# Kernel tuning notes

Hardware: AMD Instinct MI355X
Metric: run time of the kernel (lower is better)

The kernel has to match this reference:

```python
import jax, jax.numpy as jnp
import numpy as np

V, BLK, L, H, C, FF = 50257, 2048, 6, 8, 512, 2048
D = C // H  # head_dim = 64

def setup_inputs() -> dict:
    key = jax.random.key(0)
    ks = jax.random.split(key, 16)
    s = 0.02
    proj_std = 0.02 / np.sqrt(2 * L)
    return {
        'idx': jax.random.randint(ks[0], (2, 2048), 0, V, dtype=jnp.int64),
        'wte': jax.random.normal(ks[1], (V, C), jnp.float32) * s,
        'wpe': jax.random.normal(ks[2], (BLK, C), jnp.float32) * s,
        'ln1_w': jnp.ones((L, C), jnp.float32), 'ln1_b': jnp.zeros((L, C), jnp.float32),
        'c_attn_w': jax.random.normal(ks[3], (L, 3 * C, C), jnp.float32) * s,
        'c_proj_w': jax.random.normal(ks[4], (L, C, C), jnp.float32) * proj_std,
        'ln2_w': jnp.ones((L, C), jnp.float32), 'ln2_b': jnp.zeros((L, C), jnp.float32),
        'fc_w': jax.random.normal(ks[5], (L, FF, C), jnp.float32) * s,
        'proj_w': jax.random.normal(ks[6], (L, C, FF), jnp.float32) * proj_std,
        'lnf_w': jnp.ones((C,), jnp.float32), 'lnf_b': jnp.zeros((C,), jnp.float32),
    }

def _layernorm(x, w, b, eps=1e-5):
    mu = jnp.mean(x, axis=-1, keepdims=True)
    var = jnp.var(x, axis=-1, keepdims=True)
    return (x - mu) * jax.lax.rsqrt(var + eps) * w + b

def _attn(x, attn_w, proj_w, mask):
    B, T, _ = x.shape
    qkv = jnp.einsum('btc,fc->btf', x, attn_w)  # (B,T,3C)
    q, k, v = jnp.split(qkv, 3, axis=-1)
    q = q.reshape(B, T, H, D)
    k = k.reshape(B, T, H, D)
    v = v.reshape(B, T, H, D)
    scale = 1.0 / np.sqrt(D)
    att = jnp.einsum('bthd,bshd->bhts', q, k) * scale  # (B,H,T,T)
    att = jnp.where(mask, att, -jnp.inf)
    att = jax.nn.softmax(att, axis=-1)
    y = jnp.einsum('bhts,bshd->bthd', att, v).reshape(B, T, C)
    return jnp.einsum('btc,oc->bto', y, proj_w)

def reference(idx, wte, wpe, ln1_w, ln1_b, c_attn_w, c_proj_w, ln2_w, ln2_b, fc_w, proj_w, lnf_w, lnf_b):
    B, T = idx.shape
    pos = jnp.arange(T)
    x = wte[idx] + wpe[pos]  # (B,T,C); dropout p=0
    mask = jnp.tril(jnp.ones((T, T), bool))[None, None]
    for i in range(L):
        x = x + _attn(_layernorm(x, ln1_w[i], ln1_b[i]), c_attn_w[i], c_proj_w[i], mask)
        h = _layernorm(x, ln2_w[i], ln2_b[i])
        h = jax.nn.gelu(jnp.einsum('btc,fc->btf', h, fc_w[i]), approximate=False)
        x = x + jnp.einsum('btf,cf->btc', h, proj_w[i])
    x = _layernorm(x, lnf_w, lnf_b)
    logits = jnp.einsum('btc,vc->btv', x, wte)  # tied lm_head
    return logits
```

## Files before the change

### kernel.cpp

```cpp
#include <hip/hip_runtime.h>

typedef unsigned short u16;
typedef short bf16x8 __attribute__((ext_vector_type(8)));
typedef float f32x4 __attribute__((ext_vector_type(4)));
typedef unsigned short u16x4 __attribute__((ext_vector_type(4)));
typedef unsigned short u16x8 __attribute__((ext_vector_type(8)));
typedef unsigned int u32x2 __attribute__((ext_vector_type(2)));

#define B_ 2
#define T_ 2048
#define C_ 512
#define H_ 8
#define FF_ 2048
#define L_ 6
#define V_ 50257
#define M_ (B_*T_)

__device__ __forceinline__ u16 f2b(float f) {
  union { float f; unsigned u; } v; v.f = f;
  unsigned r = v.u + 0x7FFFu + ((v.u >> 16) & 1u);
  return (u16)(r >> 16);
}
__device__ __forceinline__ float b2f(u16 u) {
  union { unsigned u; float f; } v; v.u = ((unsigned)u) << 16; return v.f;
}
__device__ __forceinline__ unsigned pk_bf16(float lo, float hi) {
  unsigned r;
  asm volatile("v_cvt_pk_bf16_f32 %0, %1, %2" : "=v"(r) : "v"(lo), "v"(hi));
  return r;
}

__device__ __forceinline__ void async16(const void* g, void* l) {
  __builtin_amdgcn_global_load_lds((const __attribute__((address_space(1))) unsigned int*)g,
                                   (__attribute__((address_space(3))) unsigned int*)l, 16, 0, 0);
}

__device__ __forceinline__ bf16x8 scale8(u16x8 v, float s) {
  union { bf16x8 b; unsigned u[4]; } r;
#pragma unroll
  for (int i = 0; i < 4; i++)
    r.u[i] = pk_bf16(b2f(v[2*i]) * s, b2f(v[2*i+1]) * s);
  return r.b;
}

__global__ void cvt_bf16_k(const f32x4* __restrict__ src, u16x4* __restrict__ dst, int n4) {
  int i = blockIdx.x * blockDim.x + threadIdx.x;
  int stride = gridDim.x * blockDim.x;
  for (; i < n4; i += stride) {
    f32x4 v = src[i];
    u16x4 o;
    o[0] = f2b(v[0]); o[1] = f2b(v[1]); o[2] = f2b(v[2]); o[3] = f2b(v[3]);
    dst[i] = o;
  }
}

__global__ void embed_k(const int* __restrict__ idx, const float* __restrict__ wte,
                        const float* __restrict__ wpe, float* __restrict__ x) {
  int t = blockIdx.x * 256 + threadIdx.x;
  int row = t >> 7;
  int c4 = t & 127;
  int tok = idx[row];
  int pos = row & (T_ - 1);
  f32x4 a = ((const f32x4*)(wte + (long)tok * C_))[c4];
  f32x4 p = ((const f32x4*)(wpe + (long)pos * C_))[c4];
  ((f32x4*)x)[t] = a + p;
}

__global__ void ln_k(const float* __restrict__ x, const float* __restrict__ w,
                     const float* __restrict__ b, u16* __restrict__ out) {
  int wv = threadIdx.x >> 6;
  int lane = threadIdx.x & 63;
  int row = blockIdx.x * 4 + wv;
  const f32x4* xr = (const f32x4*)(x + (long)row * C_);
  f32x4 v0 = xr[lane * 2], v1 = xr[lane * 2 + 1];
  float s = 0.f, s2 = 0.f;
#pragma unroll
  for (int j = 0; j < 4; j++) { s += v0[j] + v1[j]; s2 += v0[j]*v0[j] + v1[j]*v1[j]; }
#pragma unroll
  for (int off = 32; off >= 1; off >>= 1) { s += __shfl_xor(s, off); s2 += __shfl_xor(s2, off); }
  float mu = s * (1.f / C_);
  float inv = rsqrtf(s2 * (1.f / C_) - mu * mu + 1e-5f);
  const f32x4* wr = (const f32x4*)w;
  const f32x4* br = (const f32x4*)b;
  f32x4 w0 = wr[lane*2], w1 = wr[lane*2+1], b0 = br[lane*2], b1 = br[lane*2+1];
  u16x8 o;
#pragma unroll
  for (int j = 0; j < 4; j++) {
    o[j]     = f2b((v0[j] - mu) * inv * w0[j] + b0[j]);
    o[j + 4] = f2b((v1[j] - mu) * inv * w1[j] + b1[j]);
  }
  *(u16x8*)(out + (long)row * C_ + lane * 8) = o;
}

template<int EPI, int BM>
__global__ __launch_bounds__(256) void gemm_bt_k(
    const u16* __restrict__ A, const u16* __restrict__ Bw,
    u16* __restrict__ Cb, float* __restrict__ Cf,
    int N, int K, int ldc)
{
  constexpr int MT = BM / 32;
  __shared__ __align__(16) u16 sA[2][BM * 32];
  __shared__ __align__(16) u16 sB[2][128 * 32];
  const int tid = threadIdx.x;
  const int n0 = blockIdx.x * 128;
  const int m0 = blockIdx.y * BM;
  const int w = tid >> 6;
  const int lane = tid & 63;
  const int wm = (w >> 1) * (BM / 2);
  const int wn = (w & 1) * 64;
  const int g = lane >> 4;
  const int l15 = lane & 15;

  f32x4 acc[MT][4] = {};

  const int nk = K >> 5;
  int arow0 = tid >> 2, ak0 = (tid & 3) * 8;
  int c1 = tid + 256;
  int arow1 = c1 >> 2, ak1 = (c1 & 3) * 8;
  int brow0 = n0 + arow0; if (brow0 > N - 1) brow0 = N - 1;
  int brow1 = n0 + arow1; if (brow1 > N - 1) brow1 = N - 1;
  const u16* gA0 = A + (long)(m0 + arow0) * K + ak0;
  const u16* gA1 = A + (long)(m0 + arow1) * K + ak1;
  const u16* gB0 = Bw + (long)brow0 * K + ak0;
  const u16* gB1 = Bw + (long)brow1 * K + ak1;
  const int lb0 = (w * 64) * 8;
  const int lb1 = (256 + w * 64) * 8;

  auto stage = [&](int buf, int kt) {
    int ko = kt << 5;
    async16(gA0 + ko, &sA[buf][lb0]);
    if constexpr (BM == 128) async16(gA1 + ko, &sA[buf][lb1]);
    async16(gB0 + ko, &sB[buf][lb0]);
    async16(gB1 + ko, &sB[buf][lb1]);
  };

  stage(0, 0);
  __syncthreads();
  int cur = 0;
  for (int kt = 0; kt < nk; kt++) {
    if (kt + 1 < nk) stage(cur ^ 1, kt + 1);
    const u16* pa = sA[cur];
    const u16* pb = sB[cur];
    bf16x8 af[MT], bfr[4];
#pragma unroll
    for (int mt = 0; mt < MT; mt++)
      af[mt] = *(const bf16x8*)(pa + (wm + mt * 16 + l15) * 32 + g * 8);
#pragma unroll
    for (int nt = 0; nt < 4; nt++)
      bfr[nt] = *(const bf16x8*)(pb + (wn + nt * 16 + l15) * 32 + g * 8);
#pragma unroll
    for (int mt = 0; mt < MT; mt++)
#pragma unroll
      for (int nt = 0; nt < 4; nt++)
        acc[mt][nt] = __builtin_amdgcn_mfma_f32_16x16x32_bf16(af[mt], bfr[nt], acc[mt][nt], 0, 0, 0);
    __syncthreads();
    cur ^= 1;
  }

#pragma unroll
  for (int mt = 0; mt < MT; mt++) {
    int m = m0 + wm + mt * 16 + g * 4;
#pragma unroll
    for (int nt = 0; nt < 4; nt++) {
      int n = n0 + wn + nt * 16 + l15;
      f32x4 v = acc[mt][nt];
#pragma unroll
      for (int r = 0; r < 4; r++) {
        long ci = (long)(m + r) * ldc + n;
        if (EPI == 0) {
          Cb[ci] = f2b(v[r]);
        } else if (EPI == 1) {
          Cf[ci] += v[r];
        } else {
          float f = v[r];
          f = 0.5f * f * (1.0f + erff(f * 0.70710678118654752f));
          Cb[ci] = f2b(f);
        }
      }
    }
  }
}

__global__ __launch_bounds__(512) void gemm_lmhead_k(
    const u16* __restrict__ A, const u16* __restrict__ Bw,
    float* __restrict__ Cf, int N)
{
  __shared__ __align__(16) u16 sA[2][256 * 32];
  __shared__ __align__(16) u16 sB[2][128 * 32];
  const int K = 512;
  const int nwg = gridDim.x;
  const int cpx = nwg >> 3;
  const int bid = blockIdx.x;
  const int swz = (bid & 7) * cpx + (bid >> 3);
  const int ntiles = (N + 127) >> 7;
  const int n0 = (swz % ntiles) * 128;
  const int m0 = (swz / ntiles) * 256;
  const int tid = threadIdx.x;
  const int w = tid >> 6;
  const int lane = tid & 63;
  const int wm = (w >> 1) * 64;
  const int wn = (w & 1) * 64;
  const int g = lane >> 4;
  const int l15 = lane & 15;

  f32x4 acc[4][4] = {};

  const int ac1 = tid + 512;
  const u16* gA0 = A + (long)(m0 + (tid >> 2)) * K + (tid & 3) * 8;
  const u16* gA1 = A + (long)(m0 + (ac1 >> 2)) * K + (ac1 & 3) * 8;
  int brow = n0 + (tid >> 2); if (brow > N - 1) brow = N - 1;
  const u16* gB0 = Bw + (long)brow * K + (tid & 3) * 8;
  const int lbA0 = (w * 64) * 8;
  const int lbA1 = (512 + w * 64) * 8;
  const int lbB0 = (w * 64) * 8;

  auto stage = [&](int buf, int kt) {
    int ko = kt << 5;
    async16(gA0 + ko, &sA[buf][lbA0]);
    async16(gA1 + ko, &sA[buf][lbA1]);
    async16(gB0 + ko, &sB[buf][lbB0]);
  };

  stage(0, 0);
  __syncthreads();
  int cur = 0;
  const int nk = K >> 5;
  for (int kt = 0; kt < nk; kt++) {
    if (kt + 1 < nk) stage(cur ^ 1, kt + 1);
    const u16* pa = sA[cur];
    const u16* pb = sB[cur];
    bf16x8 af[4], bfr[4];
#pragma unroll
    for (int mt = 0; mt < 4; mt++)
      af[mt] = *(const bf16x8*)(pa + (wm + mt * 16 + l15) * 32 + g * 8);
#pragma unroll
    for (int nt = 0; nt < 4; nt++)
      bfr[nt] = *(const bf16x8*)(pb + (wn + nt * 16 + l15) * 32 + g * 8);
#pragma unroll
    for (int mt = 0; mt < 4; mt++)
#pragma unroll
      for (int nt = 0; nt < 4; nt++)
        acc[mt][nt] = __builtin_amdgcn_mfma_f32_16x16x32_bf16(af[mt], bfr[nt], acc[mt][nt], 0, 0, 0);
    __syncthreads();
    cur ^= 1;
  }

#pragma unroll
  for (int mt = 0; mt < 4; mt++) {
    int m = m0 + wm + mt * 16 + g * 4;
#pragma unroll
    for (int nt = 0; nt < 4; nt++) {
      int n = n0 + wn + nt * 16 + l15;
      f32x4 v = acc[mt][nt];
      if (n < N) {
#pragma unroll
        for (int r = 0; r < 4; r++)
          Cf[(long)(m + r) * N + n] = v[r];
      }
    }
  }
}

__global__ __launch_bounds__(128) void attn_k(const u16* __restrict__ qkv, u16* __restrict__ out) {
  const int bh = blockIdx.y;
  const int b = bh >> 3;
  const int h = bh & 7;
  const int tid = threadIdx.x;
  const int wv = tid >> 6;
  const int lane = tid & 63;
  const int g = lane >> 4;
  const int l15 = lane & 15;
  const int qblk = 31 - (blockIdx.x >> 1);
  const int halfsel = blockIdx.x & 1;

  __shared__ __align__(16) u16 Ks[2][64 * 64];
  __shared__ __align__(16) u16 Vt[2][64 * 72];
  __shared__ __align__(16) u16 Ps[2][16 * 64];

  const long base = (long)b * T_ * 1536;
  const u16* kbase = qkv + base + 512 + h * 64;
  const u16* vbase = qkv + base + 1024 + h * 64;
  const int kq = tid & 15;
  const int dg = tid >> 4;
  const float qscale = 0.18033688011112042f;

  const int q0 = qblk * 64 + halfsel * 32 + wv * 16;

  const u16* qrow = qkv + base + (long)(q0 + l15) * 1536 + h * 64;
  bf16x8 qf0 = scale8(*(const u16x8*)(qrow + g * 8), qscale);
  bf16x8 qf1 = scale8(*(const u16x8*)(qrow + 32 + g * 8), qscale);

  f32x4 o[4] = {};
  float mrun[4] = {-1e30f, -1e30f, -1e30f, -1e30f};
  float lrun[4] = {0.f, 0.f, 0.f, 0.f};
  const int kvend = qblk * 64 + 64;

  u16x8 vreg[4];
#pragma unroll
  for (int i = 0; i < 4; i++) {
    int chunk = i * 128 + tid;
    int row = chunk >> 3, c8 = chunk & 7;
    async16(kbase + (long)row * 1536 + (c8 ^ (row & 7)) * 8,
            &Ks[0][(i * 128 + wv * 64) * 8]);
  }
#pragma unroll
  for (int t = 0; t < 4; t++)
    vreg[t] = *(const u16x8*)(vbase + (long)(kq + 16 * t) * 1536 + dg * 8);
#pragma unroll
  for (int e = 0; e < 8; e++) {
    int d = dg * 8 + e;
    u32x2 wq = { (unsigned)vreg[0][e] | ((unsigned)vreg[1][e] << 16),
                 (unsigned)vreg[2][e] | ((unsigned)vreg[3][e] << 16) };
    *(u32x2*)(&Vt[0][d * 72 + kq * 4]) = wq;
  }
  __syncthreads();

  int cur = 0;
  for (int j0 = 0; j0 < kvend; j0 += 64, cur ^= 1) {
    const bool more = (j0 + 64) < kvend;
    if (more) {
      int jn = j0 + 64;
#pragma unroll
      for (int i = 0; i < 4; i++) {
        int chunk = i * 128 + tid;
        int row = chunk >> 3, c8 = chunk & 7;
        async16(kbase + (long)(jn + row) * 1536 + (c8 ^ (row & 7)) * 8,
                &Ks[cur ^ 1][(i * 128 + wv * 64) * 8]);
      }
#pragma unroll
      for (int t = 0; t < 4; t++)
        vreg[t] = *(const u16x8*)(vbase + (long)(jn + kq + 16 * t) * 1536 + dg * 8);
    }

    f32x4 s[4] = {};
    const u16* kp = Ks[cur];
#pragma unroll
    for (int t = 0; t < 4; t++) {
      int row = t * 16 + l15;
      const u16* kr = kp + row * 64;
      bf16x8 k0 = *(const bf16x8*)(kr + ((g ^ (row & 7)) * 8));
      bf16x8 k1 = *(const bf16x8*)(kr + (((4 + g) ^ (row & 7)) * 8));
      s[t] = __builtin_amdgcn_mfma_f32_16x16x32_bf16(qf0, k0, s[t], 0, 0, 0);
      s[t] = __builtin_amdgcn_mfma_f32_16x16x32_bf16(qf1, k1, s[t], 0, 0, 0);
    }

    const bool diag = (j0 + 64) == kvend;
    u16* pw = Ps[wv];
#pragma unroll
    for (int r = 0; r < 4; r++) {
      int row = q0 + g * 4 + r;
      float v0 = s[0][r], v1 = s[1][r], v2 = s[2][r], v3 = s[3][r];
      if (diag) {
        if (j0 +      l15 > row) v0 = -1e30f;
        if (j0 + 16 + l15 > row) v1 = -1e30f;
        if (j0 + 32 + l15 > row) v2 = -1e30f;
        if (j0 + 48 + l15 > row) v3 = -1e30f;
      }
      float mloc = fmaxf(fmaxf(v0, v1), fmaxf(v2, v3));
      float m = mrun[r];
      if (!__all(mloc <= m + 8.0f)) {
        float mx = mloc;
        mx = fmaxf(mx, __shfl_xor(mx, 1));
        mx = fmaxf(mx, __shfl_xor(mx, 2));
        mx = fmaxf(mx, __shfl_xor(mx, 4));
        mx = fmaxf(mx, __shfl_xor(mx, 8));
        float mn = fmaxf(m, mx);
        float sc2 = exp2f(m - mn);
        lrun[r] *= sc2;
#pragma unroll
        for (int dt = 0; dt < 4; dt++) o[dt][r] *= sc2;
        m = mn; mrun[r] = mn;
      }
      float e0 = exp2f(v0 - m), e1 = exp2f(v1 - m);
      float e2 = exp2f(v2 - m), e3 = exp2f(v3 - m);
      lrun[r] += (e0 + e1) + (e2 + e3);
      u32x2 pkq = { pk_bf16(e0, e1), pk_bf16(e2, e3) };
      int prow = g * 4 + r;
      int byt = prow * 128 + ((((l15 >> 1) ^ (prow & 7)) << 4)) + (l15 & 1) * 8;
      *(u32x2*)((char*)pw + byt) = pkq;
    }

    const u16* vt = Vt[cur];
    bf16x8 pf0 = *(const bf16x8*)((char*)pw + l15 * 128 + (((g) ^ (l15 & 7)) << 4));
    bf16x8 pf1 = *(const bf16x8*)((char*)pw + l15 * 128 + (((4 + g) ^ (l15 & 7)) << 4));
#pragma unroll
    for (int dt = 0; dt < 4; dt++) {
      int d = dt * 16 + l15;
      bf16x8 vf0 = *(const bf16x8*)(vt + d * 72 + g * 8);
      bf16x8 vf1 = *(const bf16x8*)(vt + d * 72 + 32 + g * 8);
      o[dt] = __builtin_amdgcn_mfma_f32_16x16x32_bf16(pf0, vf0, o[dt], 0, 0, 0);
      o[dt] = __builtin_amdgcn_mfma_f32_16x16x32_bf16(pf1, vf1, o[dt], 0, 0, 0);
    }

    if (more) {
#pragma unroll
      for (int e = 0; e < 8; e++) {
        int d = dg * 8 + e;
        u32x2 wq = { (unsigned)vreg[0][e] | ((unsigned)vreg[1][e] << 16),
                     (unsigned)vreg[2][e] | ((unsigned)vreg[3][e] << 16) };
        *(u32x2*)(&Vt[cur ^ 1][d * 72 + kq * 4]) = wq;
      }
    }
    __syncthreads();
  }

#pragma unroll
  for (int r = 0; r < 4; r++) {
    float ls = lrun[r];
    ls += __shfl_xor(ls, 1); ls += __shfl_xor(ls, 2);
    ls += __shfl_xor(ls, 4); ls += __shfl_xor(ls, 8);
    float inv = 1.0f / ls;
    int row = q0 + g * 4 + r;
    u16* orow = out + (long)(b * T_ + row) * C_ + h * 64;
#pragma unroll
    for (int dt = 0; dt < 4; dt++)
      orow[dt * 16 + l15] = f2b(o[dt][r] * inv);
  }
}

extern "C" void kernel_launch(void* const* d_in, const int* in_sizes, int n_in,
                              void* d_out, int out_size, void* d_ws, size_t ws_size,
                              hipStream_t stream) {
  const int*   idx    = (const int*)  d_in[0];
  const float* wte    = (const float*)d_in[1];
  const float* wpe    = (const float*)d_in[2];
  const float* ln1w   = (const float*)d_in[3];
  const float* ln1b   = (const float*)d_in[4];
  const float* wattn  = (const float*)d_in[5];
  const float* wcproj = (const float*)d_in[6];
  const float* ln2w   = (const float*)d_in[7];
  const float* ln2b   = (const float*)d_in[8];
  const float* wfc    = (const float*)d_in[9];
  const float* wproj2 = (const float*)d_in[10];
  const float* lnfw   = (const float*)d_in[11];
  const float* lnfb   = (const float*)d_in[12];
  float* out = (float*)d_out;

  char* p = (char*)d_ws;
  size_t off = 0;
  auto alloc = [&](size_t bytes) -> void* {
    void* r = p + off; off += (bytes + 255) & ~(size_t)255; return r;
  };
  float* x    = (float*)alloc((size_t)M_ * C_ * 4);
  u16* xn     = (u16*)alloc((size_t)M_ * C_ * 2);
  u16* qkvb   = (u16*)alloc((size_t)M_ * 3 * C_ * 2);
  u16* attb   = (u16*)alloc((size_t)M_ * C_ * 2);
  u16* hb     = (u16*)alloc((size_t)M_ * FF_ * 2);
  u16* wteB   = (u16*)alloc((size_t)V_ * C_ * 2);
  u16* wattnB = (u16*)alloc((size_t)L_ * 3 * C_ * C_ * 2);
  u16* wprojB = (u16*)alloc((size_t)L_ * C_ * C_ * 2);
  u16* wfcB   = (u16*)alloc((size_t)L_ * FF_ * C_ * 2);
  u16* wp2B   = (u16*)alloc((size_t)L_ * C_ * FF_ * 2);
  if (off > ws_size) return;

  auto cvt = [&](const float* s, u16* d, long n) {
    int n4 = (int)(n >> 2);
    int blocks = (n4 + 255) / 256; if (blocks > 4096) blocks = 4096;
    cvt_bf16_k<<<dim3(blocks), dim3(256), 0, stream>>>((const f32x4*)s, (u16x4*)d, n4);
  };
  cvt(wte, wteB, (long)V_ * C_);
  cvt(wattn, wattnB, (long)L_ * 3 * C_ * C_);
  cvt(wcproj, wprojB, (long)L_ * C_ * C_);
  cvt(wfc, wfcB, (long)L_ * FF_ * C_);
  cvt(wproj2, wp2B, (long)L_ * C_ * FF_);

  embed_k<<<dim3(M_ * C_ / 4 / 256), dim3(256), 0, stream>>>(idx, wte, wpe, x);

  for (int l = 0; l < L_; l++) {
    ln_k<<<dim3(M_ / 4), dim3(256), 0, stream>>>(x, ln1w + l * C_, ln1b + l * C_, xn);
    gemm_bt_k<0, 64><<<dim3(12, 64), dim3(256), 0, stream>>>(
        xn, wattnB + (size_t)l * 3 * C_ * C_, qkvb, nullptr, 3 * C_, C_, 3 * C_);
    attn_k<<<dim3(64, B_ * H_), dim3(128), 0, stream>>>(qkvb, attb);
    gemm_bt_k<1, 64><<<dim3(4, 64), dim3(256), 0, stream>>>(
        attb, wprojB + (size_t)l * C_ * C_, nullptr, x, C_, C_, C_);
    ln_k<<<dim3(M_ / 4), dim3(256), 0, stream>>>(x, ln2w + l * C_, ln2b + l * C_, xn);
    gemm_bt_k<2, 128><<<dim3(16, 32), dim3(256), 0, stream>>>(
        xn, wfcB + (size_t)l * FF_ * C_, hb, nullptr, FF_, C_, FF_);
    gemm_bt_k<1, 64><<<dim3(4, 64), dim3(256), 0, stream>>>(
        hb, wp2B + (size_t)l * C_ * FF_, nullptr, x, C_, FF_, C_);
  }
  ln_k<<<dim3(M_ / 4), dim3(256), 0, stream>>>(x, lnfw, lnfb, xn);
  gemm_lmhead_k<<<dim3(((V_ + 127) / 128) * (M_ / 256)), dim3(512), 0, stream>>>(
      xn, wteB, out, V_);
}
```

Baseline: 1.422 ms.

## Deepen GEMM prefetch, enlarge LM-head tiles, fuse weight conversions into one launch

```diff
diff --git a/kernel.cpp b/kernel.cpp
--- a/kernel.cpp
+++ b/kernel.cpp
@@ -43,14 +43,21 @@
   return r.b;
 }
 
-__global__ void cvt_bf16_k(const f32x4* __restrict__ src, u16x4* __restrict__ dst, int n4) {
-  int i = blockIdx.x * blockDim.x + threadIdx.x;
+struct CvtArgs { const f32x4* s[5]; u16x4* d[5]; };
+__global__ void cvt_all_k(CvtArgs a) {
+  const int sizes[5] = { V_*C_/4, L_*3*C_*C_/4, L_*C_*C_/4, L_*FF_*C_/4, L_*C_*FF_/4 };
+  int gid = blockIdx.x * blockDim.x + threadIdx.x;
   int stride = gridDim.x * blockDim.x;
-  for (; i < n4; i += stride) {
-    f32x4 v = src[i];
-    u16x4 o;
-    o[0] = f2b(v[0]); o[1] = f2b(v[1]); o[2] = f2b(v[2]); o[3] = f2b(v[3]);
-    dst[i] = o;
+#pragma unroll
+  for (int seg = 0; seg < 5; seg++) {
+    const f32x4* src = a.s[seg];
+    u16x4* dst = a.d[seg];
+    for (int i = gid; i < sizes[seg]; i += stride) {
+      f32x4 v = src[i];
+      u16x4 o;
+      o[0] = f2b(v[0]); o[1] = f2b(v[1]); o[2] = f2b(v[2]); o[3] = f2b(v[3]);
+      dst[i] = o;
+    }
   }
 }
 
@@ -117,12 +124,10 @@
   int arow0 = tid >> 2, ak0 = (tid & 3) * 8;
   int c1 = tid + 256;
   int arow1 = c1 >> 2, ak1 = (c1 & 3) * 8;
-  int brow0 = n0 + arow0; if (brow0 > N - 1) brow0 = N - 1;
-  int brow1 = n0 + arow1; if (brow1 > N - 1) brow1 = N - 1;
   const u16* gA0 = A + (long)(m0 + arow0) * K + ak0;
   const u16* gA1 = A + (long)(m0 + arow1) * K + ak1;
-  const u16* gB0 = Bw + (long)brow0 * K + ak0;
-  const u16* gB1 = Bw + (long)brow1 * K + ak1;
+  const u16* gB0 = Bw + (long)(n0 + arow0) * K + ak0;
+  const u16* gB1 = Bw + (long)(n0 + arow1) * K + ak1;
   const int lb0 = (w * 64) * 8;
   const int lb1 = (256 + w * 64) * 8;
 
@@ -135,10 +140,16 @@
   };
 
   stage(0, 0);
-  __syncthreads();
-  int cur = 0;
+  stage(1, 1);
   for (int kt = 0; kt < nk; kt++) {
-    if (kt + 1 < nk) stage(cur ^ 1, kt + 1);
+    const int cur = kt & 1;
+    if (kt + 1 < nk) {
+      if constexpr (BM == 128) asm volatile("s_waitcnt vmcnt(4)" ::: "memory");
+      else                     asm volatile("s_waitcnt vmcnt(3)" ::: "memory");
+    } else {
+      asm volatile("s_waitcnt vmcnt(0)" ::: "memory");
+    }
+    __builtin_amdgcn_s_barrier();
     const u16* pa = sA[cur];
     const u16* pb = sB[cur];
     bf16x8 af[MT], bfr[4];
@@ -153,8 +164,8 @@
 #pragma unroll
       for (int nt = 0; nt < 4; nt++)
         acc[mt][nt] = __builtin_amdgcn_mfma_f32_16x16x32_bf16(af[mt], bfr[nt], acc[mt][nt], 0, 0, 0);
-    __syncthreads();
-    cur ^= 1;
+    __builtin_amdgcn_s_barrier();
+    if (kt + 2 < nk) stage(cur, kt + 2);
   }
 
 #pragma unroll
@@ -181,72 +192,74 @@
   }
 }
 
-__global__ __launch_bounds__(512) void gemm_lmhead_k(
+__global__ __launch_bounds__(512, 2) void gemm_lmhead_k(
     const u16* __restrict__ A, const u16* __restrict__ Bw,
     float* __restrict__ Cf, int N)
 {
-  __shared__ __align__(16) u16 sA[2][256 * 32];
+  __shared__ __align__(16) u16 sA[2][512 * 32];
   __shared__ __align__(16) u16 sB[2][128 * 32];
   const int K = 512;
-  const int nwg = gridDim.x;
-  const int cpx = nwg >> 3;
   const int bid = blockIdx.x;
-  const int swz = (bid & 7) * cpx + (bid >> 3);
-  const int ntiles = (N + 127) >> 7;
-  const int n0 = (swz % ntiles) * 128;
-  const int m0 = (swz / ntiles) * 256;
+  const int swz = (bid & 7) * 393 + (bid >> 3);
+  const int n0 = (swz % 393) * 128;
+  const int m0 = (swz / 393) * 512;
   const int tid = threadIdx.x;
   const int w = tid >> 6;
   const int lane = tid & 63;
-  const int wm = (w >> 1) * 64;
+  const int wm = (w >> 1) * 128;
   const int wn = (w & 1) * 64;
   const int g = lane >> 4;
   const int l15 = lane & 15;
 
-  f32x4 acc[4][4] = {};
-
-  const int ac1 = tid + 512;
-  const u16* gA0 = A + (long)(m0 + (tid >> 2)) * K + (tid & 3) * 8;
-  const u16* gA1 = A + (long)(m0 + (ac1 >> 2)) * K + (ac1 & 3) * 8;
+  f32x4 acc[8][4] = {};
+
+  const u16* gA[4];
+#pragma unroll
+  for (int i = 0; i < 4; i++) {
+    int c = tid + i * 512;
+    gA[i] = A + (long)(m0 + (c >> 2)) * K + (c & 3) * 8;
+  }
   int brow = n0 + (tid >> 2); if (brow > N - 1) brow = N - 1;
   const u16* gB0 = Bw + (long)brow * K + (tid & 3) * 8;
-  const int lbA0 = (w * 64) * 8;
-  const int lbA1 = (512 + w * 64) * 8;
-  const int lbB0 = (w * 64) * 8;
 
   auto stage = [&](int buf, int kt) {
     int ko = kt << 5;
-    async16(gA0 + ko, &sA[buf][lbA0]);
-    async16(gA1 + ko, &sA[buf][lbA1]);
-    async16(gB0 + ko, &sB[buf][lbB0]);
+#pragma unroll
+    for (int i = 0; i < 4; i++)
+      async16(gA[i] + ko, &sA[buf][(i * 512 + w * 64) * 8]);
+    async16(gB0 + ko, &sB[buf][(w * 64) * 8]);
   };
 
   stage(0, 0);
-  __syncthreads();
-  int cur = 0;
+  stage(1, 1);
   const int nk = K >> 5;
   for (int kt = 0; kt < nk; kt++) {
-    if (kt + 1 < nk) stage(cur ^ 1, kt + 1);
+    const int cur = kt & 1;
+    if (kt + 1 < nk) asm volatile("s_waitcnt vmcnt(5)" ::: "memory");
+    else             asm volatile("s_waitcnt vmcnt(0)" ::: "memory");
+    __builtin_amdgcn_s_barrier();
     const u16* pa = sA[cur];
     const u16* pb = sB[cur];
-    bf16x8 af[4], bfr[4];
-#pragma unroll
-    for (int mt = 0; mt < 4; mt++)
+    bf16x8 af[8], bfr[4];
+#pragma unroll
+    for (int mt = 0; mt < 8; mt++)
       af[mt] = *(const bf16x8*)(pa + (wm + mt * 16 + l15) * 32 + g * 8);
 #pragma unroll
     for (int nt = 0; nt < 4; nt++)
       bfr[nt] = *(const bf16x8*)(pb + (wn + nt * 16 + l15) * 32 + g * 8);
-#pragma unroll
-    for (int mt = 0; mt < 4; mt++)
+    __builtin_amdgcn_s_setprio(1);
+#pragma unroll
+    for (int mt = 0; mt < 8; mt++)
 #pragma unroll
       for (int nt = 0; nt < 4; nt++)
         acc[mt][nt] = __builtin_amdgcn_mfma_f32_16x16x32_bf16(af[mt], bfr[nt], acc[mt][nt], 0, 0, 0);
-    __syncthreads();
-    cur ^= 1;
-  }
-
-#pragma unroll
-  for (int mt = 0; mt < 4; mt++) {
+    __builtin_amdgcn_s_setprio(0);
+    __builtin_amdgcn_s_barrier();
+    if (kt + 2 < nk) stage(cur, kt + 2);
+  }
+
+#pragma unroll
+  for (int mt = 0; mt < 8; mt++) {
     int m = m0 + wm + mt * 16 + g * 4;
 #pragma unroll
     for (int nt = 0; nt < 4; nt++) {
@@ -453,16 +466,13 @@
   u16* wp2B   = (u16*)alloc((size_t)L_ * C_ * FF_ * 2);
   if (off > ws_size) return;
 
-  auto cvt = [&](const float* s, u16* d, long n) {
-    int n4 = (int)(n >> 2);
-    int blocks = (n4 + 255) / 256; if (blocks > 4096) blocks = 4096;
-    cvt_bf16_k<<<dim3(blocks), dim3(256), 0, stream>>>((const f32x4*)s, (u16x4*)d, n4);
-  };
-  cvt(wte, wteB, (long)V_ * C_);
-  cvt(wattn, wattnB, (long)L_ * 3 * C_ * C_);
-  cvt(wcproj, wprojB, (long)L_ * C_ * C_);
-  cvt(wfc, wfcB, (long)L_ * FF_ * C_);
-  cvt(wproj2, wp2B, (long)L_ * C_ * FF_);
+  CvtArgs ca;
+  ca.s[0] = (const f32x4*)wte;    ca.d[0] = (u16x4*)wteB;
+  ca.s[1] = (const f32x4*)wattn;  ca.d[1] = (u16x4*)wattnB;
+  ca.s[2] = (const f32x4*)wcproj; ca.d[2] = (u16x4*)wprojB;
+  ca.s[3] = (const f32x4*)wfc;    ca.d[3] = (u16x4*)wfcB;
+  ca.s[4] = (const f32x4*)wproj2; ca.d[4] = (u16x4*)wp2B;
+  cvt_all_k<<<dim3(2048), dim3(256), 0, stream>>>(ca);
 
   embed_k<<<dim3(M_ * C_ / 4 / 256), dim3(256), 0, stream>>>(idx, wte, wpe, x);
 
@@ -480,6 +490,5 @@
         hb, wp2B + (size_t)l * C_ * FF_, nullptr, x, C_, FF_, C_);
   }
   ln_k<<<dim3(M_ / 4), dim3(256), 0, stream>>>(x, lnfw, lnfb, xn);
-  gemm_lmhead_k<<<dim3(((V_ + 127) / 128) * (M_ / 256)), dim3(512), 0, stream>>>(
-      xn, wteB, out, V_);
-}
+  gemm_lmhead_k<<<dim3(8 * 393), dim3(512), 0, stream>>>(xn, wteB, out, V_);
+}
```

Measured after the change: 1.447 ms. Within noise of the previous version (+1.8%).
